# Kernel optimization log

Hardware: AMD Instinct MI355X
Metric: run time of the kernel (lower is better)

## Reference

```python
import jax, jax.numpy as jnp
import numpy as np

N = 131072   # octree nodes at this depth
K = 27       # 3x3x3 kernel taps
CIN = 32
COUT = 32
EPS = 1e-5   # BatchNorm1d default eps


def setup_inputs() -> dict:
    key = jax.random.key(0)
    k1, k2, k3, k4, k5 = jax.random.split(key, 5)
    data = jax.random.normal(k1, (N, CIN), dtype=jnp.float32)
    # deconv weight: one [Cin, Cout] matrix per kernel tap
    weight = jax.random.normal(k2, (K, CIN, COUT), dtype=jnp.float32) * 0.05
    gamma = 1.0 + 0.1 * jax.random.normal(k3, (COUT,), dtype=jnp.float32)
    beta = 0.1 * jax.random.normal(k4, (COUT,), dtype=jnp.float32)
    # octree neighbor table: for each input node, the K output nodes it scatters into
    neigh = jax.random.randint(k5, (N, K), 0, N, dtype=jnp.int32)
    return {"data": data, "weight": weight, "gamma": gamma, "beta": beta, "neigh": neigh}


def reference(data, weight, gamma, beta, neigh):
    # Sparse transposed conv (stride=1): each node i produces a contribution
    # data[i] @ weight[k] that is scatter-added into output node neigh[i, k].
    contrib = jnp.einsum('ni,kio->nko', data, weight)          # [N, K, Cout]
    out = jax.ops.segment_sum(contrib.reshape(-1, COUT),
                              neigh.reshape(-1),
                              num_segments=N)                   # [N, Cout]
    # BatchNorm1d (training mode: batch statistics over the node dimension)
    mean = jnp.mean(out, axis=0)
    var = jnp.var(out, axis=0)
    y = gamma * (out - mean) * jax.lax.rsqrt(var + EPS) + beta
    # ReLU
    return jnp.maximum(y, 0.0)
```

## Files before the change

kernel.cpp:

```cpp
#include <hip/hip_runtime.h>
#include <hip/hip_bf16.h>
#include <hip/hip_fp16.h>

#define NN 131072
#define KK 27
#define CC 32
#define EPSV 1e-5f

#define WS_STATS 0
#define WS_WPERM 256
#define WS_ACC   65536
#define WS_NEEDED ((size_t)WS_ACC + (size_t)NN * CC * 2)

typedef __bf16 bf16x8 __attribute__((ext_vector_type(8)));
typedef short s16x8 __attribute__((ext_vector_type(8)));
typedef float f32x4 __attribute__((ext_vector_type(4)));

__device__ inline unsigned short f2bf(float f) {
    unsigned int u = __float_as_uint(f);
    u += 0x7FFF + ((u >> 16) & 1);
    return (unsigned short)(u >> 16);
}

__global__ __launch_bounds__(256) void prep_weights_kernel(
    const float* __restrict__ weight, unsigned short* __restrict__ wperm)
{
    const int p = blockIdx.x * 256 + threadIdx.x;
    if (p >= KK * 1024) return;
    const int k  = p >> 10;
    const int ci = (p >> 5) & 31;
    const int c  = p & 31;
    const unsigned short v = f2bf(weight[p]);
    const int chalf = c & 1;
    const int col   = c >> 1;
    const int fl = col | ((ci >> 3) << 4);
    const int j = ci & 7;
    wperm[(((k << 1) | chalf) * 64 + fl) * 8 + j] = v;
}

__global__ __launch_bounds__(256) void scatter_kernel(
    const float* __restrict__ data, const unsigned short* __restrict__ wperm,
    const int* __restrict__ neigh, __half2* __restrict__ acc2)
{
    const int tid = threadIdx.x;
    const int lane = tid & 63;
    const int wv = tid >> 6;
    const int node_base = blockIdx.x * 128 + wv * 32;

    const int quad = lane >> 4;
    const int m = lane & 15;
    const int rq = quad << 2;

    s16x8 afr[2];
    #pragma unroll
    for (int g = 0; g < 2; ++g) {
        const int node = node_base + g * 16 + m;
        const float* src = data + node * 32 + quad * 8;
        const float4 v0 = *(const float4*)(src);
        const float4 v1 = *(const float4*)(src + 4);
        s16x8 s;
        s[0] = (short)f2bf(v0.x); s[1] = (short)f2bf(v0.y);
        s[2] = (short)f2bf(v0.z); s[3] = (short)f2bf(v0.w);
        s[4] = (short)f2bf(v1.x); s[5] = (short)f2bf(v1.y);
        s[6] = (short)f2bf(v1.z); s[7] = (short)f2bf(v1.w);
        afr[g] = s;
    }

    const s16x8* wp = (const s16x8*)wperm;
    const f32x4 zero = {0.f, 0.f, 0.f, 0.f};

    int nj0[4], nj1[4];
    #pragma unroll
    for (int r = 0; r < 4; ++r) {
        nj0[r] = neigh[(node_base + rq + r) * KK];
        nj1[r] = neigh[(node_base + 16 + rq + r) * KK];
    }
    s16x8 bs0 = wp[lane];
    s16x8 bs1 = wp[64 + lane];

    for (int k = 0; k < KK; ++k) {
        const int kn = (k < KK - 1) ? k + 1 : k;
        int nn0[4], nn1[4];
        #pragma unroll
        for (int r = 0; r < 4; ++r) {
            nn0[r] = neigh[(node_base + rq + r) * KK + kn];
            nn1[r] = neigh[(node_base + 16 + rq + r) * KK + kn];
        }
        const s16x8 nbs0 = wp[(kn * 2) * 64 + lane];
        const s16x8 nbs1 = wp[(kn * 2 + 1) * 64 + lane];

        {
            const f32x4 d0 = __builtin_amdgcn_mfma_f32_16x16x32_bf16(
                __builtin_bit_cast(bf16x8, afr[0]), __builtin_bit_cast(bf16x8, bs0),
                zero, 0, 0, 0);
            const f32x4 d1 = __builtin_amdgcn_mfma_f32_16x16x32_bf16(
                __builtin_bit_cast(bf16x8, afr[0]), __builtin_bit_cast(bf16x8, bs1),
                zero, 0, 0, 0);
            #pragma unroll
            for (int r = 0; r < 4; ++r) {
                __half2 v;
                v.x = __float2half(d0[r]);
                v.y = __float2half(d1[r]);
                unsafeAtomicAdd(&acc2[nj0[r] * 16 + m], v);
            }
        }
        {
            const f32x4 d0 = __builtin_amdgcn_mfma_f32_16x16x32_bf16(
                __builtin_bit_cast(bf16x8, afr[1]), __builtin_bit_cast(bf16x8, bs0),
                zero, 0, 0, 0);
            const f32x4 d1 = __builtin_amdgcn_mfma_f32_16x16x32_bf16(
                __builtin_bit_cast(bf16x8, afr[1]), __builtin_bit_cast(bf16x8, bs1),
                zero, 0, 0, 0);
            #pragma unroll
            for (int r = 0; r < 4; ++r) {
                __half2 v;
                v.x = __float2half(d0[r]);
                v.y = __float2half(d1[r]);
                unsafeAtomicAdd(&acc2[nj1[r] * 16 + m], v);
            }
        }

        bs0 = nbs0; bs1 = nbs1;
        #pragma unroll
        for (int r = 0; r < 4; ++r) { nj0[r] = nn0[r]; nj1[r] = nn1[r]; }
    }
}

__global__ __launch_bounds__(256) void stats_kernel(
    const __half2* __restrict__ acc2, float* __restrict__ stats)
{
    __shared__ float ls[16][33], ls2[16][33];
    const int tid = threadIdx.x;
    const int c2 = tid & 15, rg = tid >> 4;
    float sx = 0.f, sy = 0.f, s2x = 0.f, s2y = 0.f;
    const int row0 = blockIdx.x * 512;
    for (int it = 0; it < 32; ++it) {
        const __half2 h = acc2[(row0 + it * 16 + rg) * 16 + c2];
        const float vx = __half2float(h.x), vy = __half2float(h.y);
        sx += vx; sy += vy; s2x += vx * vx; s2y += vy * vy;
    }
    ls[rg][2 * c2] = sx;  ls[rg][2 * c2 + 1] = sy;
    ls2[rg][2 * c2] = s2x; ls2[rg][2 * c2 + 1] = s2y;
    __syncthreads();
    if (tid < 32) {
        float S = 0.f, S2 = 0.f;
        #pragma unroll
        for (int g = 0; g < 16; ++g) { S += ls[g][tid]; S2 += ls2[g][tid]; }
        atomicAdd(&stats[tid], S);
        atomicAdd(&stats[32 + tid], S2);
    }
}

__global__ __launch_bounds__(256) void bn_relu_kernel(
    const __half2* __restrict__ acc2, float* __restrict__ out,
    const float* __restrict__ stats,
    const float* __restrict__ gamma, const float* __restrict__ beta)
{
    __shared__ float sc[32], sh[32];
    const int tid = threadIdx.x;
    if (tid < 32) {
        const float mean = stats[tid] * (1.0f / NN);
        const float var  = stats[32 + tid] * (1.0f / NN) - mean * mean;
        const float s = gamma[tid] * rsqrtf(var + EPSV);
        sc[tid] = s;
        sh[tid] = beta[tid] - mean * s;
    }
    __syncthreads();
    const int idx = blockIdx.x * 256 + tid;
    const int c0 = (idx & 3) << 3;
    const __half2 h4[4] = { acc2[idx * 4], acc2[idx * 4 + 1],
                            acc2[idx * 4 + 2], acc2[idx * 4 + 3] };
    float4 o0, o1;
    o0.x = fmaxf(__half2float(h4[0].x) * sc[c0]     + sh[c0],     0.f);
    o0.y = fmaxf(__half2float(h4[0].y) * sc[c0 + 1] + sh[c0 + 1], 0.f);
    o0.z = fmaxf(__half2float(h4[1].x) * sc[c0 + 2] + sh[c0 + 2], 0.f);
    o0.w = fmaxf(__half2float(h4[1].y) * sc[c0 + 3] + sh[c0 + 3], 0.f);
    o1.x = fmaxf(__half2float(h4[2].x) * sc[c0 + 4] + sh[c0 + 4], 0.f);
    o1.y = fmaxf(__half2float(h4[2].y) * sc[c0 + 5] + sh[c0 + 5], 0.f);
    o1.z = fmaxf(__half2float(h4[3].x) * sc[c0 + 6] + sh[c0 + 6], 0.f);
    o1.w = fmaxf(__half2float(h4[3].y) * sc[c0 + 7] + sh[c0 + 7], 0.f);
    ((float4*)out)[idx * 2]     = o0;
    ((float4*)out)[idx * 2 + 1] = o1;
}

__global__ __launch_bounds__(256) void scatter_f32_kernel(
    const float* __restrict__ data, const float* __restrict__ weight,
    const int* __restrict__ neigh, float* __restrict__ out)
{
    __shared__ unsigned short wfrag[KK * 2 * 64 * 8];
    const int tid = threadIdx.x;
    const int lane = tid & 63;
    const int wv = tid >> 6;
    const int node_base = blockIdx.x * 128;
    for (int p = tid; p < KK * 1024; p += 256) {
        const int k  = p >> 10;
        const int ci = (p >> 5) & 31;
        const int c  = p & 31;
        const unsigned short v = f2bf(weight[p]);
        const int chalf = c >> 4;
        const int fl = (c & 15) | ((ci >> 3) << 4);
        const int j = ci & 7;
        wfrag[(((k << 1) | chalf) * 64 + fl) * 8 + j] = v;
    }
    const int quad = lane >> 4;
    const int m = lane & 15;
    s16x8 afr[2];
    #pragma unroll
    for (int g = 0; g < 2; ++g) {
        const int node = node_base + wv * 32 + g * 16 + m;
        const float* src = data + node * 32 + quad * 8;
        const float4 v0 = *(const float4*)(src);
        const float4 v1 = *(const float4*)(src + 4);
        s16x8 s;
        s[0] = (short)f2bf(v0.x); s[1] = (short)f2bf(v0.y);
        s[2] = (short)f2bf(v0.z); s[3] = (short)f2bf(v0.w);
        s[4] = (short)f2bf(v1.x); s[5] = (short)f2bf(v1.y);
        s[6] = (short)f2bf(v1.z); s[7] = (short)f2bf(v1.w);
        afr[g] = s;
    }
    __syncthreads();
    const int rq = quad << 2;
    const f32x4 zero = {0.f, 0.f, 0.f, 0.f};
    for (int k = 0; k < KK; ++k) {
        int nj[2][4];
        #pragma unroll
        for (int g = 0; g < 2; ++g)
            #pragma unroll
            for (int r = 0; r < 4; ++r) {
                const int node = node_base + wv * 32 + g * 16 + rq + r;
                nj[g][r] = neigh[node * KK + k];
            }
        #pragma unroll
        for (int ch = 0; ch < 2; ++ch) {
            const s16x8 bs = *(const s16x8*)&wfrag[((((k << 1) | ch)) * 64 + lane) * 8];
            const bf16x8 bfr = __builtin_bit_cast(bf16x8, bs);
            const int c = (ch << 4) | m;
            #pragma unroll
            for (int g = 0; g < 2; ++g) {
                f32x4 a2 = __builtin_amdgcn_mfma_f32_16x16x32_bf16(
                    __builtin_bit_cast(bf16x8, afr[g]), bfr, zero, 0, 0, 0);
                #pragma unroll
                for (int r = 0; r < 4; ++r)
                    __hip_atomic_fetch_add(&out[nj[g][r] * 32 + c], a2[r],
                                           __ATOMIC_RELAXED, __HIP_MEMORY_SCOPE_AGENT);
            }
        }
    }
}

__global__ __launch_bounds__(256) void stats_f32_kernel(
    const float* __restrict__ out, float* __restrict__ stats)
{
    __shared__ float ls[256], ls2[256];
    const int tid = threadIdx.x;
    const int c = tid & 31, rg = tid >> 5;
    float s = 0.f, s2 = 0.f;
    const int row0 = blockIdx.x * 512;
    for (int it = 0; it < 64; ++it) {
        const float v = out[(row0 + it * 8 + rg) * 32 + c];
        s += v; s2 += v * v;
    }
    ls[tid] = s; ls2[tid] = s2;
    __syncthreads();
    if (tid < 32) {
        float S = 0.f, S2 = 0.f;
        #pragma unroll
        for (int r = 0; r < 8; ++r) { S += ls[r * 32 + tid]; S2 += ls2[r * 32 + tid]; }
        atomicAdd(&stats[tid], S);
        atomicAdd(&stats[32 + tid], S2);
    }
}

__global__ __launch_bounds__(256) void bn_relu_f32_kernel(
    float* __restrict__ out, const float* __restrict__ stats,
    const float* __restrict__ gamma, const float* __restrict__ beta)
{
    __shared__ float sc[32], sh[32];
    const int tid = threadIdx.x;
    if (tid < 32) {
        const float mean = stats[tid] * (1.0f / NN);
        const float var  = stats[32 + tid] * (1.0f / NN) - mean * mean;
        const float s = gamma[tid] * rsqrtf(var + EPSV);
        sc[tid] = s;
        sh[tid] = beta[tid] - mean * s;
    }
    __syncthreads();
    const int idx = blockIdx.x * 256 + tid;
    float4 v = ((float4*)out)[idx];
    const int cb = (idx & 7) << 2;
    v.x = fmaxf(v.x * sc[cb]     + sh[cb],     0.f);
    v.y = fmaxf(v.y * sc[cb + 1] + sh[cb + 1], 0.f);
    v.z = fmaxf(v.z * sc[cb + 2] + sh[cb + 2], 0.f);
    v.w = fmaxf(v.w * sc[cb + 3] + sh[cb + 3], 0.f);
    ((float4*)out)[idx] = v;
}

extern "C" void kernel_launch(void* const* d_in, const int* in_sizes, int n_in,
                              void* d_out, int out_size, void* d_ws, size_t ws_size,
                              hipStream_t stream) {
    const float* data   = (const float*)d_in[0];
    const float* weight = (const float*)d_in[1];
    const float* gamma  = (const float*)d_in[2];
    const float* beta   = (const float*)d_in[3];
    const int*   neigh  = (const int*)d_in[4];
    float* out = (float*)d_out;
    char* ws = (char*)d_ws;
    float* stats = (float*)(ws + WS_STATS);

    if (ws_size >= WS_NEEDED) {
        __half2* acc2 = (__half2*)(ws + WS_ACC);
        unsigned short* wperm = (unsigned short*)(ws + WS_WPERM);
        hipMemsetAsync(ws + WS_STATS, 0, 256, stream);
        hipMemsetAsync(ws + WS_ACC, 0, (size_t)NN * CC * 2, stream);
        prep_weights_kernel<<<(KK * 1024 + 255) / 256, 256, 0, stream>>>(weight, wperm);
        scatter_kernel<<<NN / 128, 256, 0, stream>>>(data, wperm, neigh, acc2);
        stats_kernel<<<NN / 512, 256, 0, stream>>>(acc2, stats);
        bn_relu_kernel<<<(NN * CC / 8) / 256, 256, 0, stream>>>(acc2, out, stats, gamma, beta);
    } else {
        hipMemsetAsync(out, 0, (size_t)NN * CC * sizeof(float), stream);
        hipMemsetAsync(stats, 0, 64 * sizeof(float), stream);
        scatter_f32_kernel<<<NN / 128, 256, 0, stream>>>(data, weight, neigh, out);
        stats_f32_kernel<<<NN / 512, 256, 0, stream>>>(out, stats);
        bn_relu_f32_kernel<<<(NN * CC / 4) / 256, 256, 0, stream>>>(out, stats, gamma, beta);
    }
}
```

Measured before the change: 271.4 us.

## Fuse zeroing with weight prep and merge stats with BN via grid barrier

Replaces the two memsets and the weight-prep kernel with one kernel that zeroes the fp16 accumulator and stats and permutes the weights. It also fuses the stats and BN/ReLU kernels into one persistent-style kernel. Each block keeps its 256 rows in shared memory and waits on a global ticket counter until all 512 blocks have added their partial sums, so the accumulator is read from global memory once instead of twice. This cuts launch overhead and one full read pass, but depends on all 512 blocks being resident at the same time to avoid deadlock.

```diff
diff --git a/kernel.cpp b/kernel.cpp
--- a/kernel.cpp
+++ b/kernel.cpp
@@ -6,11 +6,12 @@
 #define KK 27
 #define CC 32
 #define EPSV 1e-5f
+#define NSB 512
 
 #define WS_STATS 0
-#define WS_WPERM 256
-#define WS_ACC   65536
-#define WS_NEEDED ((size_t)WS_ACC + (size_t)NN * CC * 2)
+#define WS_ACC   512
+#define WS_WPERM (512 + (size_t)NN * CC * 2)
+#define WS_NEEDED (WS_WPERM + 55296)
 
 typedef __bf16 bf16x8 __attribute__((ext_vector_type(8)));
 typedef short s16x8 __attribute__((ext_vector_type(8)));
@@ -22,31 +23,34 @@
     return (unsigned short)(u >> 16);
 }
 
-__global__ __launch_bounds__(256) void prep_weights_kernel(
-    const float* __restrict__ weight, unsigned short* __restrict__ wperm)
-{
-    const int p = blockIdx.x * 256 + threadIdx.x;
-    if (p >= KK * 1024) return;
-    const int k  = p >> 10;
-    const int ci = (p >> 5) & 31;
-    const int c  = p & 31;
-    const unsigned short v = f2bf(weight[p]);
-    const int chalf = c & 1;
-    const int col   = c >> 1;
-    const int fl = col | ((ci >> 3) << 4);
-    const int j = ci & 7;
-    wperm[(((k << 1) | chalf) * 64 + fl) * 8 + j] = v;
-}
-
-__global__ __launch_bounds__(256) void scatter_kernel(
+__global__ __launch_bounds__(256) void prep_zero_kernel(
+    const float* __restrict__ weight, unsigned short* __restrict__ wperm,
+    uint4* __restrict__ accz, unsigned int* __restrict__ statz)
+{
+    const int b = blockIdx.x, tid = threadIdx.x;
+    if (b < 2048) {
+        const uint4 z = {0u, 0u, 0u, 0u};
+        accz[b * 256 + tid] = z;
+    } else {
+        const int p = (b - 2048) * 256 + tid;
+        const int k  = p >> 10;
+        const int ci = (p >> 5) & 31;
+        const int c  = p & 31;
+        const unsigned short v = f2bf(weight[p]);
+        const int chalf = c & 1;
+        const int col   = c >> 1;
+        const int fl = col | ((ci >> 3) << 4);
+        const int j = ci & 7;
+        wperm[(((k << 1) | chalf) * 64 + fl) * 8 + j] = v;
+        if (b == 2048 && tid < 128) statz[tid] = 0u;
+    }
+}
+
+__device__ inline void scatter_body(
     const float* __restrict__ data, const unsigned short* __restrict__ wperm,
-    const int* __restrict__ neigh, __half2* __restrict__ acc2)
-{
-    const int tid = threadIdx.x;
-    const int lane = tid & 63;
-    const int wv = tid >> 6;
-    const int node_base = blockIdx.x * 128 + wv * 32;
-
+    const int* __restrict__ neigh, __half2* __restrict__ acc2,
+    int node_base, int lane)
+{
     const int quad = lane >> 4;
     const int m = lane & 15;
     const int rq = quad << 2;
@@ -88,7 +92,6 @@
         }
         const s16x8 nbs0 = wp[(kn * 2) * 64 + lane];
         const s16x8 nbs1 = wp[(kn * 2 + 1) * 64 + lane];
-
         {
             const f32x4 d0 = __builtin_amdgcn_mfma_f32_16x16x32_bf16(
                 __builtin_bit_cast(bf16x8, afr[0]), __builtin_bit_cast(bf16x8, bs0),
@@ -119,28 +122,53 @@
                 unsafeAtomicAdd(&acc2[nj1[r] * 16 + m], v);
             }
         }
-
         bs0 = nbs0; bs1 = nbs1;
         #pragma unroll
         for (int r = 0; r < 4; ++r) { nj0[r] = nn0[r]; nj1[r] = nn1[r]; }
     }
 }
 
-__global__ __launch_bounds__(256) void stats_kernel(
-    const __half2* __restrict__ acc2, float* __restrict__ stats)
-{
-    __shared__ float ls[16][33], ls2[16][33];
-    const int tid = threadIdx.x;
+__global__ __launch_bounds__(256) void scatter_kernel(
+    const float* __restrict__ data, const unsigned short* __restrict__ wperm,
+    const int* __restrict__ neigh, __half2* __restrict__ acc2)
+{
+    const int tid = threadIdx.x;
+    scatter_body(data, wperm, neigh, acc2,
+                 blockIdx.x * 128 + (tid >> 6) * 32, tid & 63);
+}
+
+__global__ __launch_bounds__(256, 2) void stats_bn_kernel(
+    const __half2* __restrict__ acc2, float* __restrict__ out,
+    float* __restrict__ stats,
+    const float* __restrict__ gamma, const float* __restrict__ beta)
+{
+    __shared__ __half2 rowbuf[256][16];
+    __shared__ float ls[16][32], ls2[16][32];
+    __shared__ float sc[32], sh[32];
+    const int tid = threadIdx.x;
+    const int bb = blockIdx.x;
+
+    {
+        const uint4* src = (const uint4*)(acc2 + (size_t)bb * 256 * 16);
+        uint4* dst = (uint4*)&rowbuf[0][0];
+        #pragma unroll
+        for (int it = 0; it < 4; ++it)
+            dst[tid + it * 256] = src[tid + it * 256];
+    }
+    __syncthreads();
+
     const int c2 = tid & 15, rg = tid >> 4;
-    float sx = 0.f, sy = 0.f, s2x = 0.f, s2y = 0.f;
-    const int row0 = blockIdx.x * 512;
-    for (int it = 0; it < 32; ++it) {
-        const __half2 h = acc2[(row0 + it * 16 + rg) * 16 + c2];
-        const float vx = __half2float(h.x), vy = __half2float(h.y);
-        sx += vx; sy += vy; s2x += vx * vx; s2y += vy * vy;
-    }
-    ls[rg][2 * c2] = sx;  ls[rg][2 * c2 + 1] = sy;
-    ls2[rg][2 * c2] = s2x; ls2[rg][2 * c2 + 1] = s2y;
+    {
+        float sx = 0.f, sy = 0.f, qx = 0.f, qy = 0.f;
+        #pragma unroll
+        for (int it = 0; it < 16; ++it) {
+            const __half2 h = rowbuf[it * 16 + rg][c2];
+            const float vx = __half2float(h.x), vy = __half2float(h.y);
+            sx += vx; sy += vy; qx += vx * vx; qy += vy * vy;
+        }
+        ls[rg][2 * c2] = sx;  ls[rg][2 * c2 + 1] = sy;
+        ls2[rg][2 * c2] = qx; ls2[rg][2 * c2 + 1] = qy;
+    }
     __syncthreads();
     if (tid < 32) {
         float S = 0.f, S2 = 0.f;
@@ -149,38 +177,41 @@
         atomicAdd(&stats[tid], S);
         atomicAdd(&stats[32 + tid], S2);
     }
-}
-
-__global__ __launch_bounds__(256) void bn_relu_kernel(
-    const __half2* __restrict__ acc2, float* __restrict__ out,
-    const float* __restrict__ stats,
-    const float* __restrict__ gamma, const float* __restrict__ beta)
-{
-    __shared__ float sc[32], sh[32];
-    const int tid = threadIdx.x;
+    if (tid == 0) {
+        unsigned int* ticket = (unsigned int*)(stats + 64);
+        __hip_atomic_fetch_add(ticket, 1u, __ATOMIC_RELEASE,
+                               __HIP_MEMORY_SCOPE_AGENT);
+        while (__hip_atomic_load(ticket, __ATOMIC_ACQUIRE,
+                                 __HIP_MEMORY_SCOPE_AGENT) < NSB)
+            __builtin_amdgcn_s_sleep(8);
+    }
+    __syncthreads();
     if (tid < 32) {
-        const float mean = stats[tid] * (1.0f / NN);
-        const float var  = stats[32 + tid] * (1.0f / NN) - mean * mean;
+        const float S  = __hip_atomic_load(&stats[tid], __ATOMIC_RELAXED,
+                                           __HIP_MEMORY_SCOPE_AGENT);
+        const float S2 = __hip_atomic_load(&stats[32 + tid], __ATOMIC_RELAXED,
+                                           __HIP_MEMORY_SCOPE_AGENT);
+        const float mean = S * (1.0f / NN);
+        const float var  = S2 * (1.0f / NN) - mean * mean;
         const float s = gamma[tid] * rsqrtf(var + EPSV);
         sc[tid] = s;
         sh[tid] = beta[tid] - mean * s;
     }
     __syncthreads();
-    const int idx = blockIdx.x * 256 + tid;
-    const int c0 = (idx & 3) << 3;
-    const __half2 h4[4] = { acc2[idx * 4], acc2[idx * 4 + 1],
-                            acc2[idx * 4 + 2], acc2[idx * 4 + 3] };
-    float4 o0, o1;
-    o0.x = fmaxf(__half2float(h4[0].x) * sc[c0]     + sh[c0],     0.f);
-    o0.y = fmaxf(__half2float(h4[0].y) * sc[c0 + 1] + sh[c0 + 1], 0.f);
-    o0.z = fmaxf(__half2float(h4[1].x) * sc[c0 + 2] + sh[c0 + 2], 0.f);
-    o0.w = fmaxf(__half2float(h4[1].y) * sc[c0 + 3] + sh[c0 + 3], 0.f);
-    o1.x = fmaxf(__half2float(h4[2].x) * sc[c0 + 4] + sh[c0 + 4], 0.f);
-    o1.y = fmaxf(__half2float(h4[2].y) * sc[c0 + 5] + sh[c0 + 5], 0.f);
-    o1.z = fmaxf(__half2float(h4[3].x) * sc[c0 + 6] + sh[c0 + 6], 0.f);
-    o1.w = fmaxf(__half2float(h4[3].y) * sc[c0 + 7] + sh[c0 + 7], 0.f);
-    ((float4*)out)[idx * 2]     = o0;
-    ((float4*)out)[idx * 2 + 1] = o1;
+
+    {
+        const float s0 = sc[2 * c2], s1 = sc[2 * c2 + 1];
+        const float h0 = sh[2 * c2], h1 = sh[2 * c2 + 1];
+        #pragma unroll
+        for (int it = 0; it < 16; ++it) {
+            const int row = it * 16 + rg;
+            const __half2 h = rowbuf[row][c2];
+            float2 v;
+            v.x = fmaxf(__half2float(h.x) * s0 + h0, 0.f);
+            v.y = fmaxf(__half2float(h.y) * s1 + h1, 0.f);
+            *(float2*)(out + ((size_t)(bb * 256 + row)) * 32 + 2 * c2) = v;
+        }
+    }
 }
 
 __global__ __launch_bounds__(256) void scatter_f32_kernel(
@@ -310,15 +341,13 @@
     if (ws_size >= WS_NEEDED) {
         __half2* acc2 = (__half2*)(ws + WS_ACC);
         unsigned short* wperm = (unsigned short*)(ws + WS_WPERM);
-        hipMemsetAsync(ws + WS_STATS, 0, 256, stream);
-        hipMemsetAsync(ws + WS_ACC, 0, (size_t)NN * CC * 2, stream);
-        prep_weights_kernel<<<(KK * 1024 + 255) / 256, 256, 0, stream>>>(weight, wperm);
+        prep_zero_kernel<<<2156, 256, 0, stream>>>(
+            weight, wperm, (uint4*)(ws + WS_ACC), (unsigned int*)stats);
         scatter_kernel<<<NN / 128, 256, 0, stream>>>(data, wperm, neigh, acc2);
-        stats_kernel<<<NN / 512, 256, 0, stream>>>(acc2, stats);
-        bn_relu_kernel<<<(NN * CC / 8) / 256, 256, 0, stream>>>(acc2, out, stats, gamma, beta);
+        stats_bn_kernel<<<NSB, 256, 0, stream>>>(acc2, out, stats, gamma, beta);
     } else {
         hipMemsetAsync(out, 0, (size_t)NN * CC * sizeof(float), stream);
-        hipMemsetAsync(stats, 0, 64 * sizeof(float), stream);
+        hipMemsetAsync(ws + WS_STATS, 0, 64 * sizeof(float), stream);
         scatter_f32_kernel<<<NN / 128, 256, 0, stream>>>(data, weight, neigh, out);
         stats_f32_kernel<<<NN / 512, 256, 0, stream>>>(out, stats);
         bn_relu_f32_kernel<<<(NN * CC / 4) / 256, 256, 0, stream>>>(out, stats, gamma, beta);
```

Result: slower. 292.6 us (+7.8%).
